# Performance work log

Measured on AMD Instinct MI355X. Metric: run time of the kernel, lower is better.

The kernel has to match this reference:

```python
import jax, jax.numpy as jnp
import numpy as np

H = 4          # num_heads
MB = 4         # ttt mini_batch_size
GRP = 4        # scan_checkpoint_group_size
TTT_LR = 0.1   # ttt_base_lr
ERF_C = 0.7071067811865476   # 1/sqrt(2)
PDF_C = 0.3989422804014327   # 1/sqrt(2*pi)


def _gelu(z):
    return 0.5 * z * (1.0 + jax.scipy.special.erf(z * ERF_C))


def _gelu_grad(z):
    return 0.5 * (1.0 + jax.scipy.special.erf(z * ERF_C)) + z * jnp.exp(-0.5 * z * z) * PDF_C


def _ln(x, w, b, eps):
    mu = x.mean(-1, keepdims=True)
    var = ((x - mu) ** 2).mean(-1, keepdims=True)
    return w * (x - mu) / jnp.sqrt(var + eps) + b


def _ln_l2_bwd(z, w, b, target, eps=1e-6):
    # grad of 0.5*||LN(z; w, b) - target||^2 w.r.t. z (fused LN backward)
    mu = z.mean(-1, keepdims=True)
    var = ((z - mu) ** 2).mean(-1, keepdims=True)
    std = jnp.sqrt(var + eps)
    zhat = (z - mu) / std
    y = w * zhat + b
    g = w * (y - target)
    return (g - g.mean(-1, keepdims=True) - zhat * (g * zhat).mean(-1, keepdims=True)) / std


def _conv1d(x, w, b, pad):
    # x: [B, Cin, L], w: [Cout, Cin, K]
    y = jax.lax.conv_general_dilated(x, w, (1,), [(pad, pad)], dimension_numbers=("NCH", "OIH", "NCH"))
    return y + b[None, :, None]


def _ttt(x, wq, wk, wv, wo, W1, b1, W2, b2, lnw, lnb):
    # x: [B, L, D];  ttt_mlp fast-weight scan over mini-batches of size MB
    B, L, D = x.shape
    d = D // H
    nmb = L // MB
    ng = nmb // GRP

    def split(w):
        # [B,L,D] -> [ng, GRP, B, H, MB, d]
        return (x @ w).reshape(B, L, H, d).transpose(0, 2, 1, 3).reshape(B, H, ng, GRP, MB, d).transpose(2, 3, 0, 1, 4, 5)

    XQ, XK, XV = split(wq), split(wk), split(wv)
    lw = lnw[None, :, None, :]  # [1,H,1,d]
    lb = lnb[None, :, None, :]
    eta = TTT_LR / MB

    carry = (jnp.broadcast_to(W1, (B, H, d, 4 * d)),
             jnp.broadcast_to(b1, (B, H, 1, 4 * d)),
             jnp.broadcast_to(W2, (B, H, 4 * d, d)),
             jnp.broadcast_to(b2, (B, H, 1, d)))

    def step(c, inp):
        W1c, b1c, W2c, b2c = c
        xq, xk, xv = inp  # each [B,H,MB,d]
        Z1 = jnp.einsum('bhmd,bhdk->bhmk', xk, W1c) + b1c
        X2 = _gelu(Z1)
        Z2 = jnp.einsum('bhmk,bhkd->bhmd', X2, W2c) + b2c
        gZ2 = _ln_l2_bwd(Z2, lw, lb, xv - xk)
        gZ1 = jnp.einsum('bhmd,bhkd->bhmk', gZ2, W2c) * _gelu_grad(Z1)
        W1n = W1c - eta * jnp.einsum('bhmd,bhmk->bhdk', xk, gZ1)
        b1n = b1c - eta * gZ1.sum(2, keepdims=True)
        W2n = W2c - eta * jnp.einsum('bhmk,bhmd->bhkd', X2, gZ2)
        b2n = b2c - eta * gZ2.sum(2, keepdims=True)
        Z1q = jnp.einsum('bhmd,bhdk->bhmk', xq, W1n) + b1n
        Z2q = jnp.einsum('bhmk,bhkd->bhmd', _gelu(Z1q), W2n) + b2n
        return (W1n, b1n, W2n, b2n), xq + _ln(Z2q, lw, lb, 1e-6)

    @jax.checkpoint
    def group(c, inp_g):
        return jax.lax.scan(step, c, inp_g)

    _, out = jax.lax.scan(group, carry, (XQ, XK, XV))  # [ng,GRP,B,H,MB,d]
    out = out.transpose(2, 3, 0, 1, 4, 5).reshape(B, H, L, d).transpose(0, 2, 1, 3).reshape(B, L, D)
    return x + out @ wo


def reference(x, conv1_w, conv1_b, convs_w, convs_b, ln_w, ln_b, wq, wk, wv, wo,
              ttt_W1, ttt_b1, ttt_W2, ttt_b2, ttt_ln_w, ttt_ln_b,
              fc_w, fc_b, fc2_w, fc2_b, fc3_w, fc3_b):
    h = x.transpose(0, 2, 1)                       # [B, dim1, L]
    h = jax.nn.relu(_conv1d(h, conv1_w, conv1_b, 0))
    acts = []
    for i in range(8):
        h = jax.nn.relu(_conv1d(h, convs_w[i], convs_b[i], 1))
        acts.append(h)
    h = acts[1] + acts[3] + acts[5] + acts[7]      # x2 + x4 + x6 + x8
    h = h.transpose(0, 2, 1)                       # [B, L, dim3]
    h = _ln(h, ln_w, ln_b, 1e-5)
    h = _ttt(h, wq, wk, wv, wo, ttt_W1, ttt_b1, ttt_W2, ttt_b2, ttt_ln_w, ttt_ln_b)
    h = _ln(h, ln_w, ln_b, 1e-5)                   # module reuses self.layer_norm
    h = h @ fc_w + fc_b
    h = h @ fc2_w + fc2_b
    return h @ fc3_w + fc3_b                       # [B, L, 1]


def setup_inputs() -> dict:
    key = jax.random.key(0)
    ks = jax.random.split(key, 12)
    B, L, dim1, dim2, dim3 = 4, 1024, 64, 512, 256
    Hn, dh = 4, 64

    def n(k, shape):
        return jax.random.normal(k, shape, jnp.float32) * 0.02

    return {
        "x": jax.random.normal(ks[0], (B, L, dim1), jnp.float32),
        "conv1_w": n(ks[1], (dim3, dim1, 1)),
        "conv1_b": jnp.zeros((dim3,), jnp.float32),
        "convs_w": n(ks[2], (8, dim3, dim3, 3)),
        "convs_b": jnp.zeros((8, dim3), jnp.float32),
        "ln_w": jnp.ones((dim3,), jnp.float32),
        "ln_b": jnp.zeros((dim3,), jnp.float32),
        "wq": n(ks[3], (dim3, dim3)),
        "wk": n(ks[4], (dim3, dim3)),
        "wv": n(ks[5], (dim3, dim3)),
        "wo": n(ks[6], (dim3, dim3)),
        "ttt_W1": n(ks[7], (Hn, dh, 4 * dh)),
        "ttt_b1": jnp.zeros((Hn, 1, 4 * dh), jnp.float32),
        "ttt_W2": n(ks[8], (Hn, 4 * dh, dh)),
        "ttt_b2": jnp.zeros((Hn, 1, dh), jnp.float32),
        "ttt_ln_w": jnp.ones((Hn, dh), jnp.float32),
        "ttt_ln_b": jnp.zeros((Hn, dh), jnp.float32),
        "fc_w": n(ks[9], (dim3, dim2)),
        "fc_b": jnp.zeros((dim2,), jnp.float32),
        "fc2_w": n(ks[10], (dim2, dim1)),
        "fc2_b": jnp.zeros((dim1,), jnp.float32),
        "fc3_w": n(ks[11], (dim1, 1)),
        "fc3_b": jnp.zeros((1,), jnp.float32),
    }
```

## Files before the change

kernel.cpp:

```cpp
#include <hip/hip_runtime.h>
#include <hip/hip_bf16.h>


#define ERF_CF 0.70710678118654752f
#define PDF_CF 0.3989422804014327f
#define ETA 0.025f

typedef __attribute__((ext_vector_type(8))) short bfrag;
typedef __attribute__((ext_vector_type(4))) float f32x4;

union FB { bfrag v; unsigned short u[8]; unsigned d[4]; };

__device__ __forceinline__ float wsum(float v) {
#pragma unroll
  for (int o = 32; o > 0; o >>= 1) v += __shfl_xor(v, o, 64);
  return v;
}

__device__ __forceinline__ unsigned pack_split(float x) {
  unsigned u = __float_as_uint(x);
  unsigned hb = u & 0xFFFF0000u;
  float lf = x - __uint_as_float(hb);
  return hb | (__float_as_uint(lf) >> 16);
}
__device__ __forceinline__ float uns(unsigned short hs, unsigned short ls) {
  return __uint_as_float((unsigned)hs << 16) + __uint_as_float((unsigned)ls << 16);
}
__device__ __forceinline__ float fb_el(const FB& H, const FB& L, int e) {
  return __uint_as_float((unsigned)H.u[e] << 16) +
         __uint_as_float((unsigned)L.u[e] << 16);
}
__device__ __forceinline__ void split2(float f, unsigned short& hs, unsigned short& ls) {
  unsigned u = __float_as_uint(f);
  unsigned hb = u & 0xFFFF0000u;
  hs = (unsigned short)(u >> 16);
  ls = (unsigned short)(__float_as_uint(f - __uint_as_float(hb)) >> 16);
}
__device__ __forceinline__ f32x4 mm3(bfrag ah, bfrag al, bfrag bh, bfrag bl, f32x4 acc) {
  acc = __builtin_amdgcn_mfma_f32_16x16x32_bf16(ah, bh, acc, 0, 0, 0);
  acc = __builtin_amdgcn_mfma_f32_16x16x32_bf16(ah, bl, acc, 0, 0, 0);
  acc = __builtin_amdgcn_mfma_f32_16x16x32_bf16(al, bh, acc, 0, 0, 0);
  return acc;
}

__global__ void prep_w(const float* __restrict__ c1w, const float* __restrict__ cw,
                       float* __restrict__ wt1, float* __restrict__ wt) {
  int id = blockIdx.x * 256 + threadIdx.x;
  if (id < 16384) {
    int ci = id >> 8, co = id & 255;
    wt1[id] = c1w[co * 64 + ci];
  }
  int id2 = id - 16384;
  if (id2 >= 0 && id2 < 1572864) {
    int cv = id2 / 196608;
    int r = id2 - cv * 196608;
    int k = r >> 8, co = r & 255;
    int tt = k >> 8, ci = k & 255;
    wt[id2] = cw[((cv * 256 + co) * 256 + ci) * 3 + tt];
  }
}

__global__ void zero_halo(float* __restrict__ bufA, float* __restrict__ bufB) {
  int id = blockIdx.x * 256 + threadIdx.x;
  int c = id & 255;
  int row = (id >> 8) & 1;
  int b = (id >> 9) & 3;
  float* p = (id >> 11) ? bufB : bufA;
  p[(b * 1026 + row * 1025) * 256 + c] = 0.0f;
}

template <int BIAS, int RELU, int RES, int OST, int ACC>
__global__ __launch_bounds__(256) void gemm_k(
    const float* __restrict__ A, const float* __restrict__ Wt,
    const float* __restrict__ bias, const float* __restrict__ res,
    float* __restrict__ out, float* __restrict__ accp,
    int M, int N, int K, int lda, int haloA) {
  __shared__ float As[16][68];
  __shared__ float Bs[16][64];
  const int tid = threadIdx.x;
  const int bm = blockIdx.x * 64, bn = blockIdx.y * 64;
  const int tx = tid & 15, ty = tid >> 4;
  float acc[4][4] = {};

  for (int k0 = 0; k0 < K; k0 += 16) {
#pragma unroll
    for (int i = 0; i < 4; ++i) {
      int idx = tid + i * 256;
      int kk = idx & 15, mm = idx >> 4;
      int m = bm + mm;
      int rb = m * lda + (haloA ? ((m >> 10) << 9) : 0);
      As[kk][mm] = A[rb + k0 + kk];
    }
#pragma unroll
    for (int i = 0; i < 4; ++i) {
      int idx = tid + i * 256;
      int nn = idx & 63, kk = idx >> 6;
      Bs[kk][nn] = Wt[(k0 + kk) * N + bn + nn];
    }
    __syncthreads();
#pragma unroll
    for (int kk = 0; kk < 16; ++kk) {
      float4 av = *(const float4*)&As[kk][ty * 4];
      float4 bv = *(const float4*)&Bs[kk][tx * 4];
      float aa[4] = {av.x, av.y, av.z, av.w};
      float bb[4] = {bv.x, bv.y, bv.z, bv.w};
#pragma unroll
      for (int i = 0; i < 4; ++i)
#pragma unroll
        for (int j = 0; j < 4; ++j) acc[i][j] = fmaf(aa[i], bb[j], acc[i][j]);
    }
    __syncthreads();
  }

  const int n0 = bn + tx * 4;
#pragma unroll
  for (int i = 0; i < 4; ++i) {
    int m = bm + ty * 4 + i;
    int b_ = m >> 10, l = m & 1023;
    float v[4];
#pragma unroll
    for (int j = 0; j < 4; ++j) {
      float x = acc[i][j];
      if constexpr (BIAS) x += bias[n0 + j];
      if constexpr (RELU) x = fmaxf(x, 0.0f);
      if constexpr (RES) x += res[m * N + n0 + j];
      v[j] = x;
    }
    float4 vv = make_float4(v[0], v[1], v[2], v[3]);
    if constexpr (OST == 0) {
      *(float4*)&out[m * N + n0] = vv;
    } else if constexpr (OST == 1) {
      *(float4*)&out[(b_ * 1026 + l + 1) * 256 + n0] = vv;
    } else {
      int hq = n0 >> 6;
      int oidx = (((b_ * 4 + hq) * 1024 + l) << 6) + (n0 & 63);
      *(float4*)&out[oidx] = vv;
    }
    if constexpr (ACC == 1) {
      *(float4*)&accp[m * 256 + n0] = vv;
    } else if constexpr (ACC == 2) {
      float4 s = *(const float4*)&accp[m * 256 + n0];
      s.x += vv.x; s.y += vv.y; s.z += vv.z; s.w += vv.w;
      *(float4*)&accp[m * 256 + n0] = s;
    }
  }
}

__global__ __launch_bounds__(256) void ln_kernel(const float* __restrict__ in,
                                                 float* __restrict__ o,
                                                 const float* __restrict__ w,
                                                 const float* __restrict__ bb,
                                                 float eps) {
  int row = blockIdx.x * 4 + (threadIdx.x >> 6);
  int l = threadIdx.x & 63;
  float4 v = ((const float4*)(in + (long)row * 256))[l];
  float s = wsum(v.x + v.y + v.z + v.w);
  float mu = s * (1.0f / 256.0f);
  float dx = v.x - mu, dy = v.y - mu, dz = v.z - mu, dw = v.w - mu;
  float rstd = rsqrtf(wsum(dx * dx + dy * dy + dz * dz + dw * dw) * (1.0f / 256.0f) + eps);
  float4 wv = ((const float4*)w)[l];
  float4 bv = ((const float4*)bb)[l];
  float4 r;
  r.x = wv.x * dx * rstd + bv.x;
  r.y = wv.y * dy * rstd + bv.y;
  r.z = wv.z * dz * rstd + bv.z;
  r.w = wv.w * dw * rstd + bv.w;
  ((float4*)(o + (long)row * 256))[l] = r;
}

__global__ __launch_bounds__(512, 2) void ttt_mfma(
    const float* __restrict__ XQ, const float* __restrict__ XK,
    const float* __restrict__ XV, const float* __restrict__ W1i,
    const float* __restrict__ B1i, const float* __restrict__ W2i,
    const float* __restrict__ B2i, const float* __restrict__ LNW,
    const float* __restrict__ LNB, float* __restrict__ outp) {
  extern __shared__ char smem[];
  unsigned short* W2Hp  = (unsigned short*)smem;
  unsigned short* W2Lp  = W2Hp + 256 * 72;
  unsigned short* W2THp = W2Lp + 256 * 72;
  unsigned short* W2TLp = W2THp + 64 * 264;
  unsigned short* X2Hp  = W2TLp + 64 * 264;
  unsigned short* X2Lp  = X2Hp + 4 * 272;
  unsigned short* xkHp  = X2Lp + 4 * 272;
  unsigned short* xkLp  = xkHp + 4 * 80;
  unsigned short* xqHp  = xkLp + 4 * 80;
  unsigned short* xqLp  = xqHp + 4 * 80;
  unsigned short* gZHp  = xqLp + 4 * 80;
  unsigned short* gZLp  = gZHp + 4 * 80;
  float* X2F  = (float*)(gZLp + 4 * 80);
  float* gZ1f = X2F + 4 * 264;
  float* Z2f  = gZ1f + 1024;
  float* redS = Z2f + 256;
  float* xvL  = redS + 512;
  float* b2L  = xvL + 256;
  float* lwL  = b2L + 64;
  float* lbL  = lwL + 64;

  const int bh = blockIdx.x, b = bh >> 2, h = bh & 3;
  const int t = threadIdx.x;
  const int w8 = t >> 6;
  const int lane = t & 63;
  const int a = lane & 15, g = lane >> 4;
  const bool rowv = (a < 4), g0 = (g == 0);
  const int c0 = 32 * w8 + a;
  const int c1 = 32 * w8 + 16 + a;
  const int kh = w8 & 1;
  const int jc = (w8 >> 1) * 16 + a;

  FB zf; zf.d[0] = zf.d[1] = zf.d[2] = zf.d[3] = 0;

  FB w1h[2][2], w1l[2][2];
#pragma unroll
  for (int i = 0; i < 2; ++i) {
    int cc = 32 * w8 + i * 16 + a;
#pragma unroll
    for (int kc = 0; kc < 2; ++kc) {
#pragma unroll
      for (int e = 0; e < 8; ++e) {
        int k = kc * 32 + g * 8 + e;
        unsigned p = pack_split(W1i[(h * 64 + k) * 256 + cc]);
        w1h[i][kc].u[e] = (unsigned short)(p >> 16);
        w1l[i][kc].u[e] = (unsigned short)(p & 0xFFFFu);
      }
    }
  }
  float b1r0 = B1i[h * 256 + c0];
  float b1r1 = B1i[h * 256 + c1];

  for (int i = 0; i < 32; ++i) {
    int id = t + i * 512;
    int k = id >> 6, j = id & 63;
    unsigned p = pack_split(W2i[(h * 256 + k) * 64 + j]);
    W2Hp[k * 72 + j] = (unsigned short)(p >> 16);
    W2Lp[k * 72 + j] = (unsigned short)(p & 0xFFFFu);
    int j2 = id >> 8, k2 = id & 255;
    unsigned q = pack_split(W2i[(h * 256 + k2) * 64 + j2]);
    W2THp[j2 * 264 + k2] = (unsigned short)(q >> 16);
    W2TLp[j2 * 264 + k2] = (unsigned short)(q & 0xFFFFu);
  }
  if (t < 64) { b2L[t] = B2i[h * 64 + t]; lwL[t] = LNW[h * 64 + t]; lbL[t] = LNB[h * 64 + t]; }

  const long chain = (long)bh * 65536;
  float rk = 0.f, rv = 0.f, rq = 0.f;
  if (t >= 256) {
    int u = t - 256;
    rk = XK[chain + u]; rv = XV[chain + u]; rq = XQ[chain + u];
  }

  for (int n = 0; n < 256; ++n) {
    if (t >= 256) {
      int u = t - 256, m = u >> 6, k = u & 63;
      unsigned short hs, ls;
      split2(rk, hs, ls); xkHp[m * 80 + k] = hs; xkLp[m * 80 + k] = ls;
      split2(rq, hs, ls); xqHp[m * 80 + k] = hs; xqLp[m * 80 + k] = ls;
      xvL[u] = rv;
    }
    __syncthreads();

    float gpA[4] = {0.f, 0.f, 0.f, 0.f}, gpB[4] = {0.f, 0.f, 0.f, 0.f};

    {
      f32x4 A0 = (f32x4){b1r0, b1r0, b1r0, b1r0};
      f32x4 A1 = (f32x4){b1r1, b1r1, b1r1, b1r1};
#pragma unroll
      for (int kc = 0; kc < 2; ++kc) {
        int base = kc * 32 + g * 8;
        FB ah = zf, al = zf;
        if (rowv) {
          ah.v = *(const bfrag*)&xkHp[a * 80 + base];
          al.v = *(const bfrag*)&xkLp[a * 80 + base];
        }
        A0 = mm3(ah.v, al.v, w1h[0][kc].v, w1l[0][kc].v, A0);
        A1 = mm3(ah.v, al.v, w1h[1][kc].v, w1l[1][kc].v, A1);
      }
      if (g0) {
#pragma unroll
        for (int q = 0; q < 4; ++q) {
          float z = A0[q];
          float er = erff(z * ERF_CF);
          float hh = 0.5f * (1.0f + er);
          float x2 = z * hh;
          gpA[q] = hh + z * __expf(-0.5f * z * z) * PDF_CF;
          unsigned short hs, ls;
          split2(x2, hs, ls);
          X2Hp[q * 272 + c0] = hs; X2Lp[q * 272 + c0] = ls;
          X2F[q * 264 + c0] = x2;
          z = A1[q];
          er = erff(z * ERF_CF);
          hh = 0.5f * (1.0f + er);
          x2 = z * hh;
          gpB[q] = hh + z * __expf(-0.5f * z * z) * PDF_CF;
          split2(x2, hs, ls);
          X2Hp[q * 272 + c1] = hs; X2Lp[q * 272 + c1] = ls;
          X2F[q * 264 + c1] = x2;
        }
      }
    }
    __syncthreads();

    {
      f32x4 acc = (f32x4){0.f, 0.f, 0.f, 0.f};
#pragma unroll
      for (int k4 = 0; k4 < 4; ++k4) {
        int base = (kh * 4 + k4) * 32 + g * 8;
        FB ah = zf, al = zf, bhf, blf;
        if (rowv) {
          ah.v = *(const bfrag*)&X2Hp[a * 272 + base];
          al.v = *(const bfrag*)&X2Lp[a * 272 + base];
        }
        bhf.v = *(const bfrag*)&W2THp[jc * 264 + base];
        blf.v = *(const bfrag*)&W2TLp[jc * 264 + base];
        acc = mm3(ah.v, al.v, bhf.v, blf.v, acc);
      }
      if (g0) {
#pragma unroll
        for (int q = 0; q < 4; ++q) redS[(kh * 4 + q) * 64 + jc] = acc[q];
      }
    }
    __syncthreads();

    if (t < 256) {
      int m = w8, j = lane;
      float z2 = b2L[j] + redS[m * 64 + j] + redS[256 + m * 64 + j];
      float mu = wsum(z2) * (1.0f / 64.0f);
      float dv = z2 - mu;
      float var = wsum(dv * dv) * (1.0f / 64.0f);
      float stdv = sqrtf(var + 1e-6f);
      float zh = dv / stdv;
      float lw = lwL[j], lb = lbL[j];
      float xkf = uns(xkHp[m * 80 + j], xkLp[m * 80 + j]);
      float tgt = xvL[m * 64 + j] - xkf;
      float gg = lw * (lw * zh + lb - tgt);
      float gs = wsum(gg) * (1.0f / 64.0f);
      float gzs = wsum(gg * zh) * (1.0f / 64.0f);
      float gz2 = (gg - gs - zh * gzs) / stdv;
      unsigned short hs, ls;
      split2(gz2, hs, ls);
      gZHp[m * 80 + j] = hs; gZLp[m * 80 + j] = ls;
      Z2f[m * 64 + j] = gz2;
    } else if (n + 1 < 256) {
      int u = t - 256;
      long nb = chain + (long)(n + 1) * 256;
      rk = XK[nb + u]; rv = XV[nb + u]; rq = XQ[nb + u];
    }
    __syncthreads();

    {
      f32x4 A0 = (f32x4){0.f, 0.f, 0.f, 0.f};
      f32x4 A1 = (f32x4){0.f, 0.f, 0.f, 0.f};
#pragma unroll
      for (int kc = 0; kc < 2; ++kc) {
        int base = kc * 32 + g * 8;
        FB ah = zf, al = zf, b0h, b0l, b1h, b1l;
        if (rowv) {
          ah.v = *(const bfrag*)&gZHp[a * 80 + base];
          al.v = *(const bfrag*)&gZLp[a * 80 + base];
        }
        b0h.v = *(const bfrag*)&W2Hp[c0 * 72 + base];
        b0l.v = *(const bfrag*)&W2Lp[c0 * 72 + base];
        b1h.v = *(const bfrag*)&W2Hp[c1 * 72 + base];
        b1l.v = *(const bfrag*)&W2Lp[c1 * 72 + base];
        A0 = mm3(ah.v, al.v, b0h.v, b0l.v, A0);
        A1 = mm3(ah.v, al.v, b1h.v, b1l.v, A1);
      }
      if (g0) {
#pragma unroll
        for (int q = 0; q < 4; ++q) {
          gZ1f[q * 256 + c0] = A0[q] * gpA[q];
          gZ1f[q * 256 + c1] = A1[q] * gpB[q];
        }
      }
      {
        int jr = t & 63, kb = (t >> 6) * 32;
        float gz0 = Z2f[jr], gz1 = Z2f[64 + jr], gz2 = Z2f[128 + jr], gz3 = Z2f[192 + jr];
#pragma unroll
        for (int kk = 0; kk < 32; kk += 8) {
          int kb8 = kb + kk;
          float x0[8], x1[8], x2[8], x3[8];
          *(float4*)&x0[0] = *(const float4*)&X2F[kb8];        *(float4*)&x0[4] = *(const float4*)&X2F[kb8 + 4];
          *(float4*)&x1[0] = *(const float4*)&X2F[264 + kb8];  *(float4*)&x1[4] = *(const float4*)&X2F[264 + kb8 + 4];
          *(float4*)&x2[0] = *(const float4*)&X2F[528 + kb8];  *(float4*)&x2[4] = *(const float4*)&X2F[528 + kb8 + 4];
          *(float4*)&x3[0] = *(const float4*)&X2F[792 + kb8];  *(float4*)&x3[4] = *(const float4*)&X2F[792 + kb8 + 4];
          FB oh, ol, nh, nl;
          oh.v = *(const bfrag*)&W2THp[jr * 264 + kb8];
          ol.v = *(const bfrag*)&W2TLp[jr * 264 + kb8];
#pragma unroll
          for (int e = 0; e < 8; ++e) {
            float u = fmaf(x3[e], gz3, fmaf(x2[e], gz2, fmaf(x1[e], gz1, x0[e] * gz0)));
            float f = fmaf(-ETA, u, fb_el(oh, ol, e));
            unsigned short hs, ls;
            split2(f, hs, ls);
            nh.u[e] = hs; nl.u[e] = ls;
          }
          *(bfrag*)&W2THp[jr * 264 + kb8] = nh.v;
          *(bfrag*)&W2TLp[jr * 264 + kb8] = nl.v;
        }
      }
    }
    __syncthreads();

    {
      float gzA0 = gZ1f[c0], gzA1 = gZ1f[256 + c0], gzA2 = gZ1f[512 + c0], gzA3 = gZ1f[768 + c0];
      float gzB0 = gZ1f[c1], gzB1 = gZ1f[256 + c1], gzB2 = gZ1f[512 + c1], gzB3 = gZ1f[768 + c1];
      b1r0 = fmaf(-ETA, ((gzA0 + gzA1) + gzA2) + gzA3, b1r0);
      b1r1 = fmaf(-ETA, ((gzB0 + gzB1) + gzB2) + gzB3, b1r1);
#pragma unroll
      for (int kc = 0; kc < 2; ++kc) {
        int base = kc * 32 + g * 8;
        FB x0h, x0l, x1h, x1l, x2h, x2l, x3h, x3l;
        x0h.v = *(const bfrag*)&xkHp[base];       x0l.v = *(const bfrag*)&xkLp[base];
        x1h.v = *(const bfrag*)&xkHp[80 + base];  x1l.v = *(const bfrag*)&xkLp[80 + base];
        x2h.v = *(const bfrag*)&xkHp[160 + base]; x2l.v = *(const bfrag*)&xkLp[160 + base];
        x3h.v = *(const bfrag*)&xkHp[240 + base]; x3l.v = *(const bfrag*)&xkLp[240 + base];
#pragma unroll
        for (int e = 0; e < 8; ++e) {
          float k0 = fb_el(x0h, x0l, e), k1 = fb_el(x1h, x1l, e);
          float k2 = fb_el(x2h, x2l, e), k3 = fb_el(x3h, x3l, e);
          float uA = fmaf(k3, gzA3, fmaf(k2, gzA2, fmaf(k1, gzA1, k0 * gzA0)));
          float uB = fmaf(k3, gzB3, fmaf(k2, gzB2, fmaf(k1, gzB1, k0 * gzB0)));
          float fA = fmaf(-ETA, uA, fb_el(w1h[0][kc], w1l[0][kc], e));
          float fB = fmaf(-ETA, uB, fb_el(w1h[1][kc], w1l[1][kc], e));
          unsigned short hs, ls;
          split2(fA, hs, ls); w1h[0][kc].u[e] = hs; w1l[0][kc].u[e] = ls;
          split2(fB, hs, ls); w1h[1][kc].u[e] = hs; w1l[1][kc].u[e] = ls;
        }
      }
      {
        f32x4 A0 = (f32x4){b1r0, b1r0, b1r0, b1r0};
        f32x4 A1 = (f32x4){b1r1, b1r1, b1r1, b1r1};
#pragma unroll
        for (int kc = 0; kc < 2; ++kc) {
          int base = kc * 32 + g * 8;
          FB ah = zf, al = zf;
          if (rowv) {
            ah.v = *(const bfrag*)&xqHp[a * 80 + base];
            al.v = *(const bfrag*)&xqLp[a * 80 + base];
          }
          A0 = mm3(ah.v, al.v, w1h[0][kc].v, w1l[0][kc].v, A0);
          A1 = mm3(ah.v, al.v, w1h[1][kc].v, w1l[1][kc].v, A1);
        }
        if (g0) {
#pragma unroll
          for (int q = 0; q < 4; ++q) {
            float z = A0[q];
            float x2 = 0.5f * z * (1.0f + erff(z * ERF_CF));
            unsigned short hs, ls;
            split2(x2, hs, ls);
            X2Hp[q * 272 + c0] = hs; X2Lp[q * 272 + c0] = ls;
            z = A1[q];
            x2 = 0.5f * z * (1.0f + erff(z * ERF_CF));
            split2(x2, hs, ls);
            X2Hp[q * 272 + c1] = hs; X2Lp[q * 272 + c1] = ls;
          }
        }
      }
      {
        int kr = t & 255, jh = (t >> 8) * 32;
        float xk0 = X2F[kr], xk1 = X2F[264 + kr], xk2 = X2F[528 + kr], xk3 = X2F[792 + kr];
#pragma unroll
        for (int jj = 0; jj < 32; jj += 8) {
          int jb = jh + jj;
          float g0f[8], g1f[8], g2f[8], g3f[8];
          *(float4*)&g0f[0] = *(const float4*)&Z2f[jb];        *(float4*)&g0f[4] = *(const float4*)&Z2f[jb + 4];
          *(float4*)&g1f[0] = *(const float4*)&Z2f[64 + jb];   *(float4*)&g1f[4] = *(const float4*)&Z2f[64 + jb + 4];
          *(float4*)&g2f[0] = *(const float4*)&Z2f[128 + jb];  *(float4*)&g2f[4] = *(const float4*)&Z2f[128 + jb + 4];
          *(float4*)&g3f[0] = *(const float4*)&Z2f[192 + jb];  *(float4*)&g3f[4] = *(const float4*)&Z2f[192 + jb + 4];
          FB oh, ol, nh, nl;
          oh.v = *(const bfrag*)&W2Hp[kr * 72 + jb];
          ol.v = *(const bfrag*)&W2Lp[kr * 72 + jb];
#pragma unroll
          for (int e = 0; e < 8; ++e) {
            float u = fmaf(xk3, g3f[e], fmaf(xk2, g2f[e], fmaf(xk1, g1f[e], xk0 * g0f[e])));
            float f = fmaf(-ETA, u, fb_el(oh, ol, e));
            unsigned short hs, ls;
            split2(f, hs, ls);
            nh.u[e] = hs; nl.u[e] = ls;
          }
          *(bfrag*)&W2Hp[kr * 72 + jb] = nh.v;
          *(bfrag*)&W2Lp[kr * 72 + jb] = nl.v;
        }
      }
      if (t < 64)
        b2L[t] -= ETA * (((Z2f[t] + Z2f[64 + t]) + Z2f[128 + t]) + Z2f[192 + t]);
    }
    __syncthreads();

    {
      f32x4 acc = (f32x4){0.f, 0.f, 0.f, 0.f};
#pragma unroll
      for (int k4 = 0; k4 < 4; ++k4) {
        int base = (kh * 4 + k4) * 32 + g * 8;
        FB ah = zf, al = zf, bhf, blf;
        if (rowv) {
          ah.v = *(const bfrag*)&X2Hp[a * 272 + base];
          al.v = *(const bfrag*)&X2Lp[a * 272 + base];
        }
        bhf.v = *(const bfrag*)&W2THp[jc * 264 + base];
        blf.v = *(const bfrag*)&W2TLp[jc * 264 + base];
        acc = mm3(ah.v, al.v, bhf.v, blf.v, acc);
      }
      if (g0) {
#pragma unroll
        for (int q = 0; q < 4; ++q) redS[(kh * 4 + q) * 64 + jc] = acc[q];
      }
    }
    __syncthreads();

    if (t < 256) {
      int m = w8, j = lane;
      float z = b2L[j] + redS[m * 64 + j] + redS[256 + m * 64 + j];
      float mu = wsum(z) * (1.0f / 64.0f);
      float dv = z - mu;
      float var = wsum(dv * dv) * (1.0f / 64.0f);
      float rstd = rsqrtf(var + 1e-6f);
      float xqf = uns(xqHp[m * 80 + j], xqLp[m * 80 + j]);
      float val = lwL[j] * dv * rstd + lbL[j] + xqf;
      outp[((long)(b * 1024 + n * 4 + m)) * 256 + h * 64 + j] = val;
    }
    __syncthreads();
  }
}

__global__ __launch_bounds__(256) void fc3_kernel(const float* __restrict__ f2,
                                                  const float* __restrict__ w,
                                                  const float* __restrict__ bias,
                                                  float* __restrict__ o) {
  int m = blockIdx.x * 4 + (threadIdx.x >> 6);
  int lane = threadIdx.x & 63;
  float v = f2[m * 64 + lane] * w[lane];
  v = wsum(v);
  if (lane == 0) o[m] = v + bias[0];
}

extern "C" void kernel_launch(void* const* d_in, const int* in_sizes, int n_in,
                              void* d_out, int out_size, void* d_ws, size_t ws_size,
                              hipStream_t stream) {
  const float* x       = (const float*)d_in[0];
  const float* conv1_w = (const float*)d_in[1];
  const float* conv1_b = (const float*)d_in[2];
  const float* convs_w = (const float*)d_in[3];
  const float* convs_b = (const float*)d_in[4];
  const float* ln_w    = (const float*)d_in[5];
  const float* ln_b    = (const float*)d_in[6];
  const float* wq      = (const float*)d_in[7];
  const float* wk      = (const float*)d_in[8];
  const float* wv      = (const float*)d_in[9];
  const float* wo      = (const float*)d_in[10];
  const float* ttt_W1  = (const float*)d_in[11];
  const float* ttt_b1  = (const float*)d_in[12];
  const float* ttt_W2  = (const float*)d_in[13];
  const float* ttt_b2  = (const float*)d_in[14];
  const float* ttt_lnw = (const float*)d_in[15];
  const float* ttt_lnb = (const float*)d_in[16];
  const float* fc_w    = (const float*)d_in[17];
  const float* fc_b    = (const float*)d_in[18];
  const float* fc2_w   = (const float*)d_in[19];
  const float* fc2_b   = (const float*)d_in[20];
  const float* fc3_w   = (const float*)d_in[21];
  const float* fc3_b   = (const float*)d_in[22];

  float* ws = (float*)d_ws;
  float* wt1  = ws + 0;
  float* wt   = ws + 16384;
  float* bufA = ws + 1589248;
  float* bufB = ws + 2639872;
  float* sum4 = ws + 3690496;
  float* tln  = ws + 4739072;
  float* XQ   = ws + 5787648;
  float* XK   = ws + 6836224;
  float* XV   = ws + 7884800;
  float* tout = ws + 8933376;
  float* tfull = sum4;
  float* h2    = bufA;
  float* f1    = XQ;
  float* f2    = tout;

  const int M = 4096;
  dim3 blk(256);

  zero_halo<<<16, blk, 0, stream>>>(bufA, bufB);
  prep_w<<<6208, blk, 0, stream>>>(conv1_w, convs_w, wt1, wt);

  gemm_k<1, 1, 0, 1, 0><<<dim3(64, 4), blk, 0, stream>>>(
      x, wt1, conv1_b, nullptr, bufA, nullptr, M, 256, 64, 64, 0);

  for (int i = 0; i < 8; ++i) {
    const float* in = (i % 2 == 0) ? bufA : bufB;
    float* out = (i % 2 == 0) ? bufB : bufA;
    const float* wp = wt + (size_t)i * 196608;
    const float* bp = convs_b + i * 256;
    if (i == 1)
      gemm_k<1, 1, 0, 1, 1><<<dim3(64, 4), blk, 0, stream>>>(
          in, wp, bp, nullptr, out, sum4, M, 256, 768, 256, 1);
    else if (i == 3 || i == 5 || i == 7)
      gemm_k<1, 1, 0, 1, 2><<<dim3(64, 4), blk, 0, stream>>>(
          in, wp, bp, nullptr, out, sum4, M, 256, 768, 256, 1);
    else
      gemm_k<1, 1, 0, 1, 0><<<dim3(64, 4), blk, 0, stream>>>(
          in, wp, bp, nullptr, out, sum4, M, 256, 768, 256, 1);
  }

  ln_kernel<<<1024, blk, 0, stream>>>(sum4, tln, ln_w, ln_b, 1e-5f);

  gemm_k<0, 0, 0, 2, 0><<<dim3(64, 4), blk, 0, stream>>>(
      tln, wq, nullptr, nullptr, XQ, nullptr, M, 256, 256, 256, 0);
  gemm_k<0, 0, 0, 2, 0><<<dim3(64, 4), blk, 0, stream>>>(
      tln, wk, nullptr, nullptr, XK, nullptr, M, 256, 256, 256, 0);
  gemm_k<0, 0, 0, 2, 0><<<dim3(64, 4), blk, 0, stream>>>(
      tln, wv, nullptr, nullptr, XV, nullptr, M, 256, 256, 256, 0);

  const int TTT_LDS = 162688;
  (void)hipFuncSetAttribute((const void*)ttt_mfma,
                            hipFuncAttributeMaxDynamicSharedMemorySize, TTT_LDS);
  ttt_mfma<<<16, dim3(512), TTT_LDS, stream>>>(XQ, XK, XV, ttt_W1, ttt_b1,
                                               ttt_W2, ttt_b2, ttt_lnw, ttt_lnb,
                                               tout);

  gemm_k<0, 0, 1, 0, 0><<<dim3(64, 4), blk, 0, stream>>>(
      tout, wo, nullptr, tln, tfull, nullptr, M, 256, 256, 256, 0);

  ln_kernel<<<1024, blk, 0, stream>>>(tfull, h2, ln_w, ln_b, 1e-5f);

  gemm_k<1, 0, 0, 0, 0><<<dim3(64, 8), blk, 0, stream>>>(
      h2, fc_w, fc_b, nullptr, f1, nullptr, M, 512, 256, 256, 0);
  gemm_k<1, 0, 0, 0, 0><<<dim3(64, 1), blk, 0, stream>>>(
      f1, fc2_w, fc2_b, nullptr, f2, nullptr, M, 64, 512, 512, 0);
  fc3_kernel<<<1024, blk, 0, stream>>>(f2, fc3_w, fc3_b, (float*)d_out);
}
```

Before: 3.056 ms.

## Port all dense GEMMs to split-bf16 MFMA with hi/lo activation planes

Replaces the scalar FP32 LDS-tiled GEMM with an MFMA kernel that emulates FP32 using three bf16x3 products, and reads operands directly from global memory without shared-memory staging. Activations between layers are stored as pre-split hi/lo bf16 planes, and weights are pre-transposed and pre-split once in a combined prep kernel. LayerNorm and the TTT kernel now emit hi/lo planes as well. The aim is to move GEMM work onto matrix cores and avoid repeated splitting, at some precision cost from three-term bf16 emulation and extra workspace aliasing.

```diff
diff --git a/kernel.cpp b/kernel.cpp
--- a/kernel.cpp
+++ b/kernel.cpp
@@ -43,114 +43,152 @@
   return acc;
 }
 
-__global__ void prep_w(const float* __restrict__ c1w, const float* __restrict__ cw,
-                       float* __restrict__ wt1, float* __restrict__ wt) {
+__global__ __launch_bounds__(256) void prep_all(
+    const float* __restrict__ c1w, const float* __restrict__ cw,
+    const float* __restrict__ wq, const float* __restrict__ wk,
+    const float* __restrict__ wv, const float* __restrict__ wo_,
+    const float* __restrict__ fcw, const float* __restrict__ fc2w,
+    unsigned short* __restrict__ WH, unsigned short* __restrict__ WL) {
   int id = blockIdx.x * 256 + threadIdx.x;
+  float val;
   if (id < 16384) {
-    int ci = id >> 8, co = id & 255;
-    wt1[id] = c1w[co * 64 + ci];
-  }
-  int id2 = id - 16384;
-  if (id2 >= 0 && id2 < 1572864) {
-    int cv = id2 / 196608;
-    int r = id2 - cv * 196608;
-    int k = r >> 8, co = r & 255;
+    val = c1w[id];
+  } else if (id < 1589248) {
+    int j = id - 16384;
+    int cv = j / 196608;
+    int r = j - cv * 196608;
+    int co = r / 768;
+    int k = r - co * 768;
     int tt = k >> 8, ci = k & 255;
-    wt[id2] = cw[((cv * 256 + co) * 256 + ci) * 3 + tt];
-  }
-}
-
-__global__ void zero_halo(float* __restrict__ bufA, float* __restrict__ bufB) {
+    val = cw[((cv * 256 + co) * 256 + ci) * 3 + tt];
+  } else if (id < 1851392) {
+    int j = id - 1589248;
+    int which = j >> 16;
+    int r = j & 65535;
+    int out = r >> 8, in = r & 255;
+    const float* Wp = which == 0 ? wq : which == 1 ? wk : which == 2 ? wv : wo_;
+    val = Wp[in * 256 + out];
+  } else if (id < 1982464) {
+    int j = id - 1851392;
+    int out = j >> 8, in = j & 255;
+    val = fcw[in * 512 + out];
+  } else {
+    int j = id - 1982464;
+    int out = j >> 9, in = j & 511;
+    val = fc2w[in * 64 + out];
+  }
+  unsigned short hs, ls;
+  split2(val, hs, ls);
+  WH[id] = hs;
+  WL[id] = ls;
+}
+
+__global__ __launch_bounds__(256) void zero_halo_pl(
+    unsigned short* __restrict__ cAH, unsigned short* __restrict__ cAL,
+    unsigned short* __restrict__ cBH, unsigned short* __restrict__ cBL) {
   int id = blockIdx.x * 256 + threadIdx.x;
-  int c = id & 255;
-  int row = (id >> 8) & 1;
-  int b = (id >> 9) & 3;
-  float* p = (id >> 11) ? bufB : bufA;
-  p[(b * 1026 + row * 1025) * 256 + c] = 0.0f;
-}
-
-template <int BIAS, int RELU, int RES, int OST, int ACC>
-__global__ __launch_bounds__(256) void gemm_k(
-    const float* __restrict__ A, const float* __restrict__ Wt,
-    const float* __restrict__ bias, const float* __restrict__ res,
-    float* __restrict__ out, float* __restrict__ accp,
-    int M, int N, int K, int lda, int haloA) {
-  __shared__ float As[16][68];
-  __shared__ float Bs[16][64];
+  int buf = id >> 11;
+  int r = id & 2047;
+  int b = r >> 9, row = (r >> 8) & 1, c = r & 255;
+  unsigned short* p = buf == 0 ? cAH : buf == 1 ? cAL : buf == 2 ? cBH : cBL;
+  p[(b * 1026 + row * 1025) * 256 + c] = 0;
+}
+
+template <int AF32, int HALOA, int BIAS, int RELU, int EPI, int ACC>
+__global__ __launch_bounds__(256) void gemm_mf(
+    const unsigned short* __restrict__ AH, const unsigned short* __restrict__ AL,
+    const float* __restrict__ Af32,
+    const unsigned short* __restrict__ BH, const unsigned short* __restrict__ BL,
+    const float* __restrict__ bias,
+    const unsigned short* __restrict__ resH, const unsigned short* __restrict__ resL,
+    float* __restrict__ outF, unsigned short* __restrict__ outH,
+    unsigned short* __restrict__ outL, float* __restrict__ acc4,
+    int N, int K) {
   const int tid = threadIdx.x;
-  const int bm = blockIdx.x * 64, bn = blockIdx.y * 64;
-  const int tx = tid & 15, ty = tid >> 4;
-  float acc[4][4] = {};
-
-  for (int k0 = 0; k0 < K; k0 += 16) {
-#pragma unroll
-    for (int i = 0; i < 4; ++i) {
-      int idx = tid + i * 256;
-      int kk = idx & 15, mm = idx >> 4;
-      int m = bm + mm;
-      int rb = m * lda + (haloA ? ((m >> 10) << 9) : 0);
-      As[kk][mm] = A[rb + k0 + kk];
-    }
-#pragma unroll
-    for (int i = 0; i < 4; ++i) {
-      int idx = tid + i * 256;
-      int nn = idx & 63, kk = idx >> 6;
-      Bs[kk][nn] = Wt[(k0 + kk) * N + bn + nn];
-    }
-    __syncthreads();
-#pragma unroll
-    for (int kk = 0; kk < 16; ++kk) {
-      float4 av = *(const float4*)&As[kk][ty * 4];
-      float4 bv = *(const float4*)&Bs[kk][tx * 4];
-      float aa[4] = {av.x, av.y, av.z, av.w};
-      float bb[4] = {bv.x, bv.y, bv.z, bv.w};
-#pragma unroll
-      for (int i = 0; i < 4; ++i)
-#pragma unroll
-        for (int j = 0; j < 4; ++j) acc[i][j] = fmaf(aa[i], bb[j], acc[i][j]);
-    }
-    __syncthreads();
-  }
-
-  const int n0 = bn + tx * 4;
-#pragma unroll
-  for (int i = 0; i < 4; ++i) {
-    int m = bm + ty * 4 + i;
-    int b_ = m >> 10, l = m & 1023;
-    float v[4];
-#pragma unroll
-    for (int j = 0; j < 4; ++j) {
-      float x = acc[i][j];
-      if constexpr (BIAS) x += bias[n0 + j];
-      if constexpr (RELU) x = fmaxf(x, 0.0f);
-      if constexpr (RES) x += res[m * N + n0 + j];
-      v[j] = x;
-    }
-    float4 vv = make_float4(v[0], v[1], v[2], v[3]);
-    if constexpr (OST == 0) {
-      *(float4*)&out[m * N + n0] = vv;
-    } else if constexpr (OST == 1) {
-      *(float4*)&out[(b_ * 1026 + l + 1) * 256 + n0] = vv;
+  const int w = tid >> 6, lane = tid & 63;
+  const int a = lane & 15, g = lane >> 4;
+  const int s = w >> 1, ch = w & 1;
+  const int bm = blockIdx.x * 32, bn = blockIdx.y * 64;
+  const int rowA = bm + 16 * s + a;
+  long abase;
+  if constexpr (HALOA)
+    abase = (long)((rowA >> 10) * 1026 + (rowA & 1023)) * 256;
+  else
+    abase = (long)rowA * K;
+  const int cb0 = bn + (ch * 2) * 16 + a;
+  const int cb1 = cb0 + 16;
+  f32x4 acc0 = {0.f, 0.f, 0.f, 0.f}, acc1 = {0.f, 0.f, 0.f, 0.f};
+#pragma unroll 2
+  for (int kk = 0; kk < K; kk += 32) {
+    FB ah, al;
+    if constexpr (AF32) {
+      const float* ap = Af32 + abase + kk + g * 8;
+      float av[8];
+      *(float4*)&av[0] = *(const float4*)ap;
+      *(float4*)&av[4] = *(const float4*)(ap + 4);
+#pragma unroll
+      for (int e = 0; e < 8; ++e) split2(av[e], ah.u[e], al.u[e]);
     } else {
-      int hq = n0 >> 6;
-      int oidx = (((b_ * 4 + hq) * 1024 + l) << 6) + (n0 & 63);
-      *(float4*)&out[oidx] = vv;
-    }
-    if constexpr (ACC == 1) {
-      *(float4*)&accp[m * 256 + n0] = vv;
-    } else if constexpr (ACC == 2) {
-      float4 s = *(const float4*)&accp[m * 256 + n0];
-      s.x += vv.x; s.y += vv.y; s.z += vv.z; s.w += vv.w;
-      *(float4*)&accp[m * 256 + n0] = s;
-    }
-  }
-}
-
-__global__ __launch_bounds__(256) void ln_kernel(const float* __restrict__ in,
-                                                 float* __restrict__ o,
-                                                 const float* __restrict__ w,
-                                                 const float* __restrict__ bb,
-                                                 float eps) {
+      ah.v = *(const bfrag*)&AH[abase + kk + g * 8];
+      al.v = *(const bfrag*)&AL[abase + kk + g * 8];
+    }
+    FB b0h, b0l, b1h, b1l;
+    b0h.v = *(const bfrag*)&BH[(long)cb0 * K + kk + g * 8];
+    b0l.v = *(const bfrag*)&BL[(long)cb0 * K + kk + g * 8];
+    b1h.v = *(const bfrag*)&BH[(long)cb1 * K + kk + g * 8];
+    b1l.v = *(const bfrag*)&BL[(long)cb1 * K + kk + g * 8];
+    acc0 = mm3(ah.v, al.v, b0h.v, b0l.v, acc0);
+    acc1 = mm3(ah.v, al.v, b1h.v, b1l.v, acc1);
+  }
+#pragma unroll
+  for (int i = 0; i < 2; ++i) {
+    f32x4 av = i ? acc1 : acc0;
+    int col = i ? cb1 : cb0;
+    float bv = 0.f;
+    if constexpr (BIAS) bv = bias[col];
+#pragma unroll
+    for (int q = 0; q < 4; ++q) {
+      int r = bm + 16 * s + g * 4 + q;
+      float val = av[q] + bv;
+      if constexpr (RELU) val = fmaxf(val, 0.f);
+      if constexpr (EPI == 4) {
+        long ri = (long)r * N + col;
+        val += uns(resH[ri], resL[ri]);
+      }
+      if constexpr (EPI == 0 || EPI == 4) {
+        outF[(long)r * N + col] = val;
+      } else if constexpr (EPI == 1) {
+        long hi = (long)((r >> 10) * 1026 + (r & 1023) + 1) * 256 + col;
+        unsigned short hs, ls;
+        split2(val, hs, ls);
+        outH[hi] = hs;
+        outL[hi] = ls;
+      } else if constexpr (EPI == 2) {
+        int b_ = r >> 10, l = r & 1023, hq = col >> 6;
+        long oidx = (((long)(b_ * 4 + hq) * 1024 + l) << 6) + (col & 63);
+        outF[oidx] = val;
+      } else if constexpr (EPI == 3) {
+        long oi = (long)r * N + col;
+        unsigned short hs, ls;
+        split2(val, hs, ls);
+        outH[oi] = hs;
+        outL[oi] = ls;
+      }
+      if constexpr (ACC == 1) {
+        acc4[(long)r * 256 + col] = val;
+      } else if constexpr (ACC == 2) {
+        acc4[(long)r * 256 + col] += val;
+      }
+    }
+  }
+}
+
+__global__ __launch_bounds__(256) void ln_pl(const float* __restrict__ in,
+                                             unsigned short* __restrict__ oH,
+                                             unsigned short* __restrict__ oL,
+                                             const float* __restrict__ w,
+                                             const float* __restrict__ bb,
+                                             float eps) {
   int row = blockIdx.x * 4 + (threadIdx.x >> 6);
   int l = threadIdx.x & 63;
   float4 v = ((const float4*)(in + (long)row * 256))[l];
@@ -160,12 +198,19 @@
   float rstd = rsqrtf(wsum(dx * dx + dy * dy + dz * dz + dw * dw) * (1.0f / 256.0f) + eps);
   float4 wv = ((const float4*)w)[l];
   float4 bv = ((const float4*)bb)[l];
-  float4 r;
-  r.x = wv.x * dx * rstd + bv.x;
-  r.y = wv.y * dy * rstd + bv.y;
-  r.z = wv.z * dz * rstd + bv.z;
-  r.w = wv.w * dw * rstd + bv.w;
-  ((float4*)(o + (long)row * 256))[l] = r;
+  float rr[4];
+  rr[0] = wv.x * dx * rstd + bv.x;
+  rr[1] = wv.y * dy * rstd + bv.y;
+  rr[2] = wv.z * dz * rstd + bv.z;
+  rr[3] = wv.w * dw * rstd + bv.w;
+  long base = (long)row * 256 + l * 4;
+#pragma unroll
+  for (int j = 0; j < 4; ++j) {
+    unsigned short hs, ls;
+    split2(rr[j], hs, ls);
+    oH[base + j] = hs;
+    oL[base + j] = ls;
+  }
 }
 
 __global__ __launch_bounds__(512, 2) void ttt_mfma(
@@ -173,7 +218,8 @@
     const float* __restrict__ XV, const float* __restrict__ W1i,
     const float* __restrict__ B1i, const float* __restrict__ W2i,
     const float* __restrict__ B2i, const float* __restrict__ LNW,
-    const float* __restrict__ LNB, float* __restrict__ outp) {
+    const float* __restrict__ LNB, unsigned short* __restrict__ outH,
+    unsigned short* __restrict__ outL) {
   extern __shared__ char smem[];
   unsigned short* W2Hp  = (unsigned short*)smem;
   unsigned short* W2Lp  = W2Hp + 256 * 72;
@@ -386,8 +432,8 @@
           ol.v = *(const bfrag*)&W2TLp[jr * 264 + kb8];
 #pragma unroll
           for (int e = 0; e < 8; ++e) {
-            float u = fmaf(x3[e], gz3, fmaf(x2[e], gz2, fmaf(x1[e], gz1, x0[e] * gz0)));
-            float f = fmaf(-ETA, u, fb_el(oh, ol, e));
+            float uu = fmaf(x3[e], gz3, fmaf(x2[e], gz2, fmaf(x1[e], gz1, x0[e] * gz0)));
+            float f = fmaf(-ETA, uu, fb_el(oh, ol, e));
             unsigned short hs, ls;
             split2(f, hs, ls);
             nh.u[e] = hs; nl.u[e] = ls;
@@ -470,8 +516,8 @@
           ol.v = *(const bfrag*)&W2Lp[kr * 72 + jb];
 #pragma unroll
           for (int e = 0; e < 8; ++e) {
-            float u = fmaf(xk3, g3f[e], fmaf(xk2, g2f[e], fmaf(xk1, g1f[e], xk0 * g0f[e])));
-            float f = fmaf(-ETA, u, fb_el(oh, ol, e));
+            float uu = fmaf(xk3, g3f[e], fmaf(xk2, g2f[e], fmaf(xk1, g1f[e], xk0 * g0f[e])));
+            float f = fmaf(-ETA, uu, fb_el(oh, ol, e));
             unsigned short hs, ls;
             split2(f, hs, ls);
             nh.u[e] = hs; nl.u[e] = ls;
@@ -515,7 +561,11 @@
       float rstd = rsqrtf(var + 1e-6f);
       float xqf = uns(xqHp[m * 80 + j], xqLp[m * 80 + j]);
       float val = lwL[j] * dv * rstd + lbL[j] + xqf;
-      outp[((long)(b * 1024 + n * 4 + m)) * 256 + h * 64 + j] = val;
+      long oidx = ((long)(b * 1024 + n * 4 + m)) * 256 + h * 64 + j;
+      unsigned short hs, ls;
+      split2(val, hs, ls);
+      outH[oidx] = hs;
+      outL[oidx] = ls;
     }
     __syncthreads();
   }
@@ -559,71 +609,93 @@
   const float* fc3_w   = (const float*)d_in[21];
   const float* fc3_b   = (const float*)d_in[22];
 
-  float* ws = (float*)d_ws;
-  float* wt1  = ws + 0;
-  float* wt   = ws + 16384;
-  float* bufA = ws + 1589248;
-  float* bufB = ws + 2639872;
-  float* sum4 = ws + 3690496;
-  float* tln  = ws + 4739072;
-  float* XQ   = ws + 5787648;
-  float* XK   = ws + 6836224;
-  float* XV   = ws + 7884800;
-  float* tout = ws + 8933376;
+  unsigned short* U = (unsigned short*)d_ws;
+  unsigned short* WH   = U;
+  unsigned short* WL   = U + 2015232;
+  unsigned short* cAH  = U + 4030464;
+  unsigned short* cAL  = U + 5081088;
+  unsigned short* cBH  = U + 6131712;
+  unsigned short* cBL  = U + 7182336;
+  unsigned short* tlnH = U + 8232960;
+  unsigned short* tlnL = U + 9281536;
+  unsigned short* toH  = U + 10330112;
+  unsigned short* toL  = U + 11378688;
+  float* F = (float*)d_ws;
+  float* sum4 = F + 6213632;
+  float* XQ   = sum4;
   float* tfull = sum4;
-  float* h2    = bufA;
-  float* f1    = XQ;
-  float* f2    = tout;
-
-  const int M = 4096;
+  float* XK   = F + 7262208;
+  float* XV   = F + 8310784;
+  unsigned short* f1H = (unsigned short*)XK;
+  unsigned short* f1L = (unsigned short*)XV;
+  float* f2 = (float*)toH;
+  unsigned short* h2H = cAH;
+  unsigned short* h2L = cAL;
+
+  const int W_WT1 = 0, W_WT = 16384, W_QKVO = 1589248, W_FC = 1851392, W_FC2 = 1982464;
+
   dim3 blk(256);
 
-  zero_halo<<<16, blk, 0, stream>>>(bufA, bufB);
-  prep_w<<<6208, blk, 0, stream>>>(conv1_w, convs_w, wt1, wt);
-
-  gemm_k<1, 1, 0, 1, 0><<<dim3(64, 4), blk, 0, stream>>>(
-      x, wt1, conv1_b, nullptr, bufA, nullptr, M, 256, 64, 64, 0);
+  zero_halo_pl<<<32, blk, 0, stream>>>(cAH, cAL, cBH, cBL);
+  prep_all<<<7872, blk, 0, stream>>>(conv1_w, convs_w, wq, wk, wv, wo, fc_w,
+                                     fc2_w, WH, WL);
+
+  gemm_mf<1, 0, 1, 1, 1, 0><<<dim3(128, 4), blk, 0, stream>>>(
+      nullptr, nullptr, x, WH + W_WT1, WL + W_WT1, conv1_b, nullptr, nullptr,
+      nullptr, cAH, cAL, nullptr, 256, 64);
 
   for (int i = 0; i < 8; ++i) {
-    const float* in = (i % 2 == 0) ? bufA : bufB;
-    float* out = (i % 2 == 0) ? bufB : bufA;
-    const float* wp = wt + (size_t)i * 196608;
+    const unsigned short* iH = (i % 2 == 0) ? cAH : cBH;
+    const unsigned short* iL = (i % 2 == 0) ? cAL : cBL;
+    unsigned short* oH = (i % 2 == 0) ? cBH : cAH;
+    unsigned short* oL = (i % 2 == 0) ? cBL : cAL;
+    const unsigned short* bH = WH + W_WT + i * 196608;
+    const unsigned short* bL = WL + W_WT + i * 196608;
     const float* bp = convs_b + i * 256;
     if (i == 1)
-      gemm_k<1, 1, 0, 1, 1><<<dim3(64, 4), blk, 0, stream>>>(
-          in, wp, bp, nullptr, out, sum4, M, 256, 768, 256, 1);
+      gemm_mf<0, 1, 1, 1, 1, 1><<<dim3(128, 4), blk, 0, stream>>>(
+          iH, iL, nullptr, bH, bL, bp, nullptr, nullptr, nullptr, oH, oL, sum4,
+          256, 768);
     else if (i == 3 || i == 5 || i == 7)
-      gemm_k<1, 1, 0, 1, 2><<<dim3(64, 4), blk, 0, stream>>>(
-          in, wp, bp, nullptr, out, sum4, M, 256, 768, 256, 1);
+      gemm_mf<0, 1, 1, 1, 1, 2><<<dim3(128, 4), blk, 0, stream>>>(
+          iH, iL, nullptr, bH, bL, bp, nullptr, nullptr, nullptr, oH, oL, sum4,
+          256, 768);
     else
-      gemm_k<1, 1, 0, 1, 0><<<dim3(64, 4), blk, 0, stream>>>(
-          in, wp, bp, nullptr, out, sum4, M, 256, 768, 256, 1);
-  }
-
-  ln_kernel<<<1024, blk, 0, stream>>>(sum4, tln, ln_w, ln_b, 1e-5f);
-
-  gemm_k<0, 0, 0, 2, 0><<<dim3(64, 4), blk, 0, stream>>>(
-      tln, wq, nullptr, nullptr, XQ, nullptr, M, 256, 256, 256, 0);
-  gemm_k<0, 0, 0, 2, 0><<<dim3(64, 4), blk, 0, stream>>>(
-      tln, wk, nullptr, nullptr, XK, nullptr, M, 256, 256, 256, 0);
-  gemm_k<0, 0, 0, 2, 0><<<dim3(64, 4), blk, 0, stream>>>(
-      tln, wv, nullptr, nullptr, XV, nullptr, M, 256, 256, 256, 0);
+      gemm_mf<0, 1, 1, 1, 1, 0><<<dim3(128, 4), blk, 0, stream>>>(
+          iH, iL, nullptr, bH, bL, bp, nullptr, nullptr, nullptr, oH, oL,
+          nullptr, 256, 768);
+  }
+
+  ln_pl<<<1024, blk, 0, stream>>>(sum4, tlnH, tlnL, ln_w, ln_b, 1e-5f);
+
+  gemm_mf<0, 0, 0, 0, 2, 0><<<dim3(128, 4), blk, 0, stream>>>(
+      tlnH, tlnL, nullptr, WH + W_QKVO + 0 * 65536, WL + W_QKVO + 0 * 65536,
+      nullptr, nullptr, nullptr, XQ, nullptr, nullptr, nullptr, 256, 256);
+  gemm_mf<0, 0, 0, 0, 2, 0><<<dim3(128, 4), blk, 0, stream>>>(
+      tlnH, tlnL, nullptr, WH + W_QKVO + 1 * 65536, WL + W_QKVO + 1 * 65536,
+      nullptr, nullptr, nullptr, XK, nullptr, nullptr, nullptr, 256, 256);
+  gemm_mf<0, 0, 0, 0, 2, 0><<<dim3(128, 4), blk, 0, stream>>>(
+      tlnH, tlnL, nullptr, WH + W_QKVO + 2 * 65536, WL + W_QKVO + 2 * 65536,
+      nullptr, nullptr, nullptr, XV, nullptr, nullptr, nullptr, 256, 256);
 
   const int TTT_LDS = 162688;
   (void)hipFuncSetAttribute((const void*)ttt_mfma,
                             hipFuncAttributeMaxDynamicSharedMemorySize, TTT_LDS);
   ttt_mfma<<<16, dim3(512), TTT_LDS, stream>>>(XQ, XK, XV, ttt_W1, ttt_b1,
                                                ttt_W2, ttt_b2, ttt_lnw, ttt_lnb,
-                                               tout);
-
-  gemm_k<0, 0, 1, 0, 0><<<dim3(64, 4), blk, 0, stream>>>(
-      tout, wo, nullptr, tln, tfull, nullptr, M, 256, 256, 256, 0);
-
-  ln_kernel<<<1024, blk, 0, stream>>>(tfull, h2, ln_w, ln_b, 1e-5f);
-
-  gemm_k<1, 0, 0, 0, 0><<<dim3(64, 8), blk, 0, stream>>>(
-      h2, fc_w, fc_b, nullptr, f1, nullptr, M, 512, 256, 256, 0);
-  gemm_k<1, 0, 0, 0, 0><<<dim3(64, 1), blk, 0, stream>>>(
-      f1, fc2_w, fc2_b, nullptr, f2, nullptr, M, 64, 512, 512, 0);
+                                               toH, toL);
+
+  gemm_mf<0, 0, 0, 0, 4, 0><<<dim3(128, 4), blk, 0, stream>>>(
+      toH, toL, nullptr, WH + W_QKVO + 3 * 65536, WL + W_QKVO + 3 * 65536,
+      nullptr, tlnH, tlnL, tfull, nullptr, nullptr, nullptr, 256, 256);
+
+  ln_pl<<<1024, blk, 0, stream>>>(tfull, h2H, h2L, ln_w, ln_b, 1e-5f);
+
+  gemm_mf<0, 0, 1, 0, 3, 0><<<dim3(128, 8), blk, 0, stream>>>(
+      h2H, h2L, nullptr, WH + W_FC, WL + W_FC, fc_b, nullptr, nullptr, nullptr,
+      f1H, f1L, nullptr, 512, 256);
+  gemm_mf<0, 0, 1, 0, 0, 0><<<dim3(128, 1), blk, 0, stream>>>(
+      f1H, f1L, nullptr, WH + W_FC2, WL + W_FC2, fc2_b, nullptr, nullptr, f2,
+      nullptr, nullptr, nullptr, 64, 512);
   fc3_kernel<<<1024, blk, 0, stream>>>(f2, fc3_w, fc3_b, (float*)d_out);
 }
```

Measured after the change: 2.931 ms. 1.04x faster.
